# Performance work log

Measured on AMD Instinct MI355X. Metric: run time of the kernel, lower is better.

Reference implementation:

```python
import jax, jax.numpy as jnp
import numpy as np

BN_EPS = 1e-5
NUM_HEADS = 16


def setup_inputs() -> dict:
    key = jax.random.key(0)
    k1, k2 = jax.random.split(key)
    B, F, E = 8, 1024, 1024
    x = jax.random.normal(k1, (B, F, E), dtype=jnp.float32)
    # xavier_uniform for Linear(E, 3E): bound = sqrt(6/(E + 3E))
    bound = float(np.sqrt(6.0 / (E + 3 * E)))
    W_qkv = jax.random.uniform(k2, (3 * E, E), minval=-bound, maxval=bound, dtype=jnp.float32)
    b_qkv = jnp.zeros((3 * E,), dtype=jnp.float32)
    gamma = jnp.ones((F,), dtype=jnp.float32)
    beta = jnp.zeros((F,), dtype=jnp.float32)
    return {"x": x, "gamma": gamma, "beta": beta, "W_qkv": W_qkv, "b_qkv": b_qkv}


def reference(x, gamma, beta, W_qkv, b_qkv):
    B, F, E = x.shape
    H = NUM_HEADS
    hd = E // H
    # BatchNorm1d(features_dim) in training mode: channels = F axis,
    # stats over (batch, embed) dims, biased variance.
    mean = jnp.mean(x, axis=(0, 2), keepdims=True)          # [1,F,1]
    var = jnp.mean((x - mean) ** 2, axis=(0, 2), keepdims=True)
    xn = (x - mean) * jax.lax.rsqrt(var + BN_EPS)
    xn = xn * gamma[None, :, None] + beta[None, :, None]
    # QKV projection: torch Linear -> xn @ W^T + b
    qkv = jnp.einsum('bfe,oe->bfo', xn, W_qkv) + b_qkv       # [B,F,3E]
    qkv = qkv.reshape(B, F, H, 3 * hd).transpose(0, 2, 1, 3) # [B,H,F,3hd]
    q, k, v = jnp.split(qkv, 3, axis=-1)                     # each [B,H,F,hd]
    scale = 1.0 / jnp.sqrt(jnp.float32(hd))
    logits = jnp.einsum('bhqd,bhkd->bhqk', q, k) * scale     # [B,H,F,F]
    attn = jax.nn.softmax(logits, axis=-1)
    values = jnp.einsum('bhqk,bhkd->bhqd', attn, v)          # [B,H,F,hd]
    values = values.transpose(0, 2, 1, 3).reshape(B, F, E)
    return values
```

## Files before the change

kernel.cpp:

```cpp
#include <hip/hip_runtime.h>

typedef unsigned short u16;
typedef unsigned int   u32;

typedef __bf16 bf16x8 __attribute__((ext_vector_type(8)));
typedef float  f32x4  __attribute__((ext_vector_type(4)));

typedef const __attribute__((address_space(1))) void* gas_ptr;
typedef __attribute__((address_space(3))) void* las_ptr;

__device__ __forceinline__ u16 f2bf(float f) {
  u32 u = __builtin_bit_cast(u32, f);
  u += 0x7fffu + ((u >> 16) & 1u);
  return (u16)(u >> 16);
}
__device__ __forceinline__ float bf2f(u16 u) {
  return __builtin_bit_cast(float, ((u32)u) << 16);
}
__device__ __forceinline__ u32 pk2(float a, float b) {
  return (u32)f2bf(a) | ((u32)f2bf(b) << 16);
}

__global__ __launch_bounds__(256) void bn_norm_kernel(
    const float* __restrict__ x, const float* __restrict__ gamma,
    const float* __restrict__ beta, u16* __restrict__ xn) {
  const int F = 1024, E = 1024;
  int f = blockIdx.x;
  __shared__ float sh[8192];
  __shared__ float ps[4], pq[4], sc[2];

  const float* xf = x + (size_t)f * E;
  float ls = 0.f, lq = 0.f;
  for (int i = threadIdx.x; i < 8192; i += 256) {
    int b = i >> 10, e = i & 1023;
    float v = xf[(size_t)b * F * E + e];
    sh[i] = v;
    ls += v;
    lq += v * v;
  }
  #pragma unroll
  for (int o = 32; o > 0; o >>= 1) {
    ls += __shfl_down(ls, o, 64);
    lq += __shfl_down(lq, o, 64);
  }
  int w = threadIdx.x >> 6;
  if ((threadIdx.x & 63) == 0) { ps[w] = ls; pq[w] = lq; }
  __syncthreads();
  if (threadIdx.x == 0) {
    float s = ps[0] + ps[1] + ps[2] + ps[3];
    float q = pq[0] + pq[1] + pq[2] + pq[3];
    float mean = s * (1.f / 8192.f);
    float var = q * (1.f / 8192.f) - mean * mean;
    float scale = gamma[f] * rsqrtf(var + 1e-5f);
    sc[0] = scale;
    sc[1] = beta[f] - mean * scale;
  }
  __syncthreads();
  float scale = sc[0], shift = sc[1];
  for (int i = threadIdx.x; i < 8192; i += 256) {
    int b = i >> 10, e = i & 1023;
    xn[((size_t)(b * F + f)) * E + e] = f2bf(sh[i] * scale + shift);
  }
}

__global__ __launch_bounds__(256) void wconv_kernel(
    const float* __restrict__ W, u16* __restrict__ Wb) {
  const int total = 3072 * 1024 / 4;
  for (int i = blockIdx.x * 256 + threadIdx.x; i < total; i += gridDim.x * 256) {
    float4 v = ((const float4*)W)[i];
    ushort4 o;
    o.x = f2bf(v.x); o.y = f2bf(v.y); o.z = f2bf(v.z); o.w = f2bf(v.w);
    ((ushort4*)Wb)[i] = o;
  }
}

__global__ __launch_bounds__(256) void gemm_qkv_kernel(
    const u16* __restrict__ A, const u16* __restrict__ Bw,
    const float* __restrict__ bias, u16* __restrict__ C) {
  const int K = 1024, N = 3072;
  __shared__ u16 As[128 * 32];
  __shared__ u16 Bs[128 * 32];

  int m0 = blockIdx.x * 128, n0 = blockIdx.y * 128;
  int t = threadIdx.x, lane = t & 63, w = t >> 6;
  int wr = w >> 1, wc = w & 1;
  int r = lane & 15, g = lane >> 4;

  int srow = t >> 2, scol = (t & 3) * 8;
  const u16* gA  = A  + (size_t)(m0 + srow) * K + scol;
  const u16* gA2 = gA + (size_t)64 * K;
  const u16* gB  = Bw + (size_t)(n0 + srow) * K + scol;
  const u16* gB2 = gB + (size_t)64 * K;
  u16* lA  = As + t * 8;
  u16* lA2 = As + 2048 + t * 8;
  u16* lB  = Bs + t * 8;
  u16* lB2 = Bs + 2048 + t * 8;

  f32x4 acc[4][4] = {};

  const u16* pA = As + (size_t)(wr * 64 + r) * 32 + g * 8;
  const u16* pB = Bs + (size_t)(wc * 64 + r) * 32 + g * 8;

  for (int k0 = 0; k0 < K; k0 += 32) {
    __builtin_amdgcn_global_load_lds((gas_ptr)gA,  (las_ptr)lA,  16, 0, 0);
    __builtin_amdgcn_global_load_lds((gas_ptr)gA2, (las_ptr)lA2, 16, 0, 0);
    __builtin_amdgcn_global_load_lds((gas_ptr)gB,  (las_ptr)lB,  16, 0, 0);
    __builtin_amdgcn_global_load_lds((gas_ptr)gB2, (las_ptr)lB2, 16, 0, 0);
    gA += 32; gA2 += 32; gB += 32; gB2 += 32;
    __syncthreads();

    bf16x8 af[4], bfr[4];
    #pragma unroll
    for (int mi = 0; mi < 4; ++mi)
      af[mi] = __builtin_bit_cast(bf16x8, *(const int4*)(pA + mi * 512));
    #pragma unroll
    for (int ni = 0; ni < 4; ++ni)
      bfr[ni] = __builtin_bit_cast(bf16x8, *(const int4*)(pB + ni * 512));
    #pragma unroll
    for (int mi = 0; mi < 4; ++mi)
      #pragma unroll
      for (int ni = 0; ni < 4; ++ni)
        acc[mi][ni] = __builtin_amdgcn_mfma_f32_16x16x32_bf16(af[mi], bfr[ni], acc[mi][ni], 0, 0, 0);
    __syncthreads();
  }

  #pragma unroll
  for (int ni = 0; ni < 4; ++ni) {
    int col = n0 + wc * 64 + ni * 16 + r;
    float bv = bias[col];
    #pragma unroll
    for (int mi = 0; mi < 4; ++mi) {
      int row = m0 + wr * 64 + mi * 16 + g * 4;
      #pragma unroll
      for (int j = 0; j < 4; ++j)
        C[(size_t)(row + j) * N + col] = f2bf(acc[mi][ni][j] + bv);
    }
  }
}

__global__ __launch_bounds__(256) void vt_kernel(
    const u16* __restrict__ qkv, u16* __restrict__ Vt) {
  __shared__ u16 T[64][72];
  int bh = blockIdx.y, b = bh >> 4, h = bh & 15;
  int f0 = blockIdx.x * 64;
  int t = threadIdx.x;
  int fl = t >> 2, c16 = (t & 3) * 16;
  const u16* src = qkv + (size_t)(b * 1024 + f0 + fl) * 3072 + h * 192 + 128 + c16;
  *(int4*)&T[fl][c16]     = *(const int4*)src;
  *(int4*)&T[fl][c16 + 8] = *(const int4*)(src + 8);
  __syncthreads();
  int dl = t >> 2, fc = (t & 3) * 16;
  u16 buf[16];
  #pragma unroll
  for (int j = 0; j < 16; ++j) {
    int c = fc + j;
    int m = c & 31;
    int a = ((m & 4) << 2) | ((m & 16) >> 1) | ((m & 8) >> 1) | (m & 3);
    buf[j] = T[(c & 32) | a][dl];
  }
  u16* dst = Vt + (size_t)bh * 65536 + (size_t)dl * 1024 + f0 + fc;
  *(int4*)dst       = *(int4*)&buf[0];
  *(int4*)(dst + 8) = *(int4*)&buf[8];
}

__global__ __launch_bounds__(256) void attn_kernel(
    const u16* __restrict__ qkv, const u16* __restrict__ Vt,
    float* __restrict__ out) {
  const int F = 1024, NQ = 3072;
  int bid = blockIdx.x;
  int xcd = bid & 7;
  int li  = bid >> 3;
  int bh  = ((li >> 4) << 3) | xcd;
  int ql  = li & 15;
  int w   = threadIdx.x >> 6;
  int lane = threadIdx.x & 63;
  int q = lane & 15, g = lane >> 4;
  int qs = q & 7;
  int q0 = ql * 64 + w * 16;
  int b = bh >> 4, h = bh & 15;

  const u16* base = qkv + (size_t)b * F * NQ + h * 192;
  const u16* VtBH = Vt + (size_t)bh * 65536;

  __shared__ u16 S[16384];

  int i8 = lane >> 3;
  int ic = lane & 7;

  const float qscale = 0.125f * 1.4426950408889634f;
  bf16x8 Qf0, Qf1;
  {
    const u16* qp = base + (size_t)(q0 + q) * NQ + g * 8;
    union { int4 v; u16 u[8]; } uu0, uu1;
    uu0.v = *(const int4*)(qp);
    uu1.v = *(const int4*)(qp + 32);
    union { u16 u[8]; bf16x8 v; } p0, p1;
    #pragma unroll
    for (int j = 0; j < 8; ++j) {
      p0.u[j] = f2bf(bf2f(uu0.u[j]) * qscale);
      p1.u[j] = f2bf(bf2f(uu1.u[j]) * qscale);
    }
    Qf0 = p0.v; Qf1 = p1.v;
  }

  f32x4 acc[4] = {};
  float m = -INFINITY, lsum = 0.f;

  #define STAGE(buf, kt)                                                       \
    do {                                                                       \
      int kb_ = (kt) * 64;                                                     \
      _Pragma("unroll")                                                        \
      for (int rr = 0; rr < 2; ++rr) {                                         \
        int r_ = rr * 32 + w * 8 + i8;                                         \
        int sc_ = (ic ^ (r_ & 7)) * 8;                                         \
        const u16* ks_ = base + (size_t)(kb_ + r_) * NQ + 64 + sc_;            \
        const u16* vs_ = VtBH + (size_t)r_ * 1024 + kb_ + sc_;                 \
        __builtin_amdgcn_global_load_lds((gas_ptr)ks_,                         \
            (las_ptr)&S[(buf) * 4096 + (rr * 32 + w * 8) * 64], 16, 0, 0);     \
        __builtin_amdgcn_global_load_lds((gas_ptr)vs_,                         \
            (las_ptr)&S[8192 + (buf) * 4096 + (rr * 32 + w * 8) * 64], 16, 0, 0);\
      }                                                                        \
    } while (0)

  STAGE(0, 0);
  __syncthreads();

  int cur = 0;
  for (int kt = 0; kt < 16; ++kt) {
    if (kt < 15) STAGE(cur ^ 1, kt + 1);

    const u16* Kb = &S[cur * 4096];
    const u16* Vb = &S[8192 + cur * 4096];

    f32x4 s[4];
    #pragma unroll
    for (int ks = 0; ks < 4; ++ks) {
      int row = ks * 16 + q;
      int4 k0 = *(const int4*)&Kb[row * 64 + ((g ^ qs) * 8)];
      int4 k1 = *(const int4*)&Kb[row * 64 + (((4 + g) ^ qs) * 8)];
      f32x4 sv = {0.f, 0.f, 0.f, 0.f};
      sv = __builtin_amdgcn_mfma_f32_16x16x32_bf16(__builtin_bit_cast(bf16x8, k0), Qf0, sv, 0, 0, 0);
      sv = __builtin_amdgcn_mfma_f32_16x16x32_bf16(__builtin_bit_cast(bf16x8, k1), Qf1, sv, 0, 0, 0);
      s[ks] = sv;
    }

    float tmx = s[0][0];
    #pragma unroll
    for (int ks = 0; ks < 4; ++ks) {
      tmx = fmaxf(tmx, fmaxf(fmaxf(s[ks][0], s[ks][1]), fmaxf(s[ks][2], s[ks][3])));
    }
    if (__any(tmx > m + 8.0f)) {
      float tr = fmaxf(tmx, __shfl_xor(tmx, 16, 64));
      tr = fmaxf(tr, __shfl_xor(tr, 32, 64));
      float mnew = fmaxf(m, tr);
      float alpha = exp2f(m - mnew);
      lsum *= alpha;
      acc[0] *= alpha; acc[1] *= alpha; acc[2] *= alpha; acc[3] *= alpha;
      m = mnew;
    }
    float p[16];
    #pragma unroll
    for (int ks = 0; ks < 4; ++ks) {
      p[ks * 4 + 0] = exp2f(s[ks][0] - m);
      p[ks * 4 + 1] = exp2f(s[ks][1] - m);
      p[ks * 4 + 2] = exp2f(s[ks][2] - m);
      p[ks * 4 + 3] = exp2f(s[ks][3] - m);
    }
    float psum = 0.f;
    #pragma unroll
    for (int j = 0; j < 16; ++j) psum += p[j];
    lsum += psum;

    union { u32 w4[4]; bf16x8 v; } pb0, pb1;
    pb0.w4[0] = pk2(p[0], p[1]);   pb0.w4[1] = pk2(p[2], p[3]);
    pb0.w4[2] = pk2(p[4], p[5]);   pb0.w4[3] = pk2(p[6], p[7]);
    pb1.w4[0] = pk2(p[8], p[9]);   pb1.w4[1] = pk2(p[10], p[11]);
    pb1.w4[2] = pk2(p[12], p[13]); pb1.w4[3] = pk2(p[14], p[15]);

    #pragma unroll
    for (int dt = 0; dt < 4; ++dt) {
      int row = dt * 16 + q;
      int4 v0 = *(const int4*)&Vb[row * 64 + ((g ^ qs) * 8)];
      int4 v1 = *(const int4*)&Vb[row * 64 + (((4 + g) ^ qs) * 8)];
      acc[dt] = __builtin_amdgcn_mfma_f32_16x16x32_bf16(__builtin_bit_cast(bf16x8, v0), pb0.v, acc[dt], 0, 0, 0);
      acc[dt] = __builtin_amdgcn_mfma_f32_16x16x32_bf16(__builtin_bit_cast(bf16x8, v1), pb1.v, acc[dt], 0, 0, 0);
    }

    __syncthreads();
    cur ^= 1;
  }
  #undef STAGE

  lsum += __shfl_xor(lsum, 16, 64);
  lsum += __shfl_xor(lsum, 32, 64);
  float inv = 1.0f / lsum;

  float* oT = (float*)S + (size_t)w * 1088;
  #pragma unroll
  for (int dt = 0; dt < 4; ++dt) {
    oT[(dt * 16 + g * 4 + 0) * 17 + q] = acc[dt][0] * inv;
    oT[(dt * 16 + g * 4 + 1) * 17 + q] = acc[dt][1] * inv;
    oT[(dt * 16 + g * 4 + 2) * 17 + q] = acc[dt][2] * inv;
    oT[(dt * 16 + g * 4 + 3) * 17 + q] = acc[dt][3] * inv;
  }
  asm volatile("s_waitcnt lgkmcnt(0)" ::: "memory");
  int oq = lane >> 2, dc = (lane & 3) * 16;
  float* orow = out + (size_t)(b * F + q0 + oq) * 1024 + h * 64 + dc;
  #pragma unroll
  for (int c4 = 0; c4 < 4; ++c4) {
    float4 v;
    v.x = oT[(dc + c4 * 4 + 0) * 17 + oq];
    v.y = oT[(dc + c4 * 4 + 1) * 17 + oq];
    v.z = oT[(dc + c4 * 4 + 2) * 17 + oq];
    v.w = oT[(dc + c4 * 4 + 3) * 17 + oq];
    *(float4*)(orow + c4 * 4) = v;
  }
}

extern "C" void kernel_launch(void* const* d_in, const int* in_sizes, int n_in,
                              void* d_out, int out_size, void* d_ws, size_t ws_size,
                              hipStream_t stream) {
  const float* x     = (const float*)d_in[0];
  const float* gamma = (const float*)d_in[1];
  const float* beta  = (const float*)d_in[2];
  const float* W     = (const float*)d_in[3];
  const float* bias  = (const float*)d_in[4];
  float* out = (float*)d_out;

  char* ws = (char*)d_ws;
  u16* xn  = (u16*)ws;
  u16* Wb  = (u16*)(ws + (size_t)16 * 1024 * 1024);
  u16* qkv = (u16*)(ws + (size_t)22 * 1024 * 1024);
  u16* Vt  = (u16*)(ws + (size_t)70 * 1024 * 1024);

  bn_norm_kernel<<<1024, 256, 0, stream>>>(x, gamma, beta, xn);
  wconv_kernel<<<768, 256, 0, stream>>>(W, Wb);
  gemm_qkv_kernel<<<dim3(64, 24), 256, 0, stream>>>(xn, Wb, bias, qkv);
  vt_kernel<<<dim3(16, 128), 256, 0, stream>>>(qkv, Vt);
  attn_kernel<<<2048, 256, 0, stream>>>(qkv, Vt, out);
}
```

Baseline: 171.5 us.

## Fold running max into MFMA accumulator seed and use hardware bf16 pack

The attention inner loop now seeds the QK MFMA accumulator with -m, so scores arrive already shifted and the per-element subtraction before exp2 disappears in the common case. The rescale branch works on the offset relative to the current max and is marked unlikely. Software bf16 rounding is replaced by the v_cvt_pk_bf16_f32 instruction, the max and sum reductions become trees, and s_setprio is raised around the MFMA blocks. Together these aim to cut VALU work in the softmax, in exchange for inline asm and a max that now starts at 0 instead of -inf.

```diff
diff --git a/kernel.cpp b/kernel.cpp
--- a/kernel.cpp
+++ b/kernel.cpp
@@ -17,8 +17,10 @@
 __device__ __forceinline__ float bf2f(u16 u) {
   return __builtin_bit_cast(float, ((u32)u) << 16);
 }
-__device__ __forceinline__ u32 pk2(float a, float b) {
-  return (u32)f2bf(a) | ((u32)f2bf(b) << 16);
+__device__ __forceinline__ u32 cvtpk(float a, float b) {
+  u32 r;
+  asm("v_cvt_pk_bf16_f32 %0, %1, %2" : "=v"(r) : "v"(a), "v"(b));
+  return r;
 }
 
 __global__ __launch_bounds__(256) void bn_norm_kernel(
@@ -194,17 +196,17 @@
     union { int4 v; u16 u[8]; } uu0, uu1;
     uu0.v = *(const int4*)(qp);
     uu1.v = *(const int4*)(qp + 32);
-    union { u16 u[8]; bf16x8 v; } p0, p1;
-    #pragma unroll
-    for (int j = 0; j < 8; ++j) {
-      p0.u[j] = f2bf(bf2f(uu0.u[j]) * qscale);
-      p1.u[j] = f2bf(bf2f(uu1.u[j]) * qscale);
+    union { u32 w4[4]; bf16x8 v; } p0, p1;
+    #pragma unroll
+    for (int j = 0; j < 4; ++j) {
+      p0.w4[j] = cvtpk(bf2f(uu0.u[2 * j]) * qscale, bf2f(uu0.u[2 * j + 1]) * qscale);
+      p1.w4[j] = cvtpk(bf2f(uu1.u[2 * j]) * qscale, bf2f(uu1.u[2 * j + 1]) * qscale);
     }
     Qf0 = p0.v; Qf1 = p1.v;
   }
 
   f32x4 acc[4] = {};
-  float m = -INFINITY, lsum = 0.f;
+  float m = 0.0f, lsum = 0.f;
 
   #define STAGE(buf, kt)                                                       \
     do {                                                                       \
@@ -233,50 +235,65 @@
     const u16* Vb = &S[8192 + cur * 4096];
 
     f32x4 s[4];
+    f32x4 seed = {-m, -m, -m, -m};
+    __builtin_amdgcn_s_setprio(1);
     #pragma unroll
     for (int ks = 0; ks < 4; ++ks) {
       int row = ks * 16 + q;
       int4 k0 = *(const int4*)&Kb[row * 64 + ((g ^ qs) * 8)];
       int4 k1 = *(const int4*)&Kb[row * 64 + (((4 + g) ^ qs) * 8)];
-      f32x4 sv = {0.f, 0.f, 0.f, 0.f};
+      f32x4 sv = seed;
       sv = __builtin_amdgcn_mfma_f32_16x16x32_bf16(__builtin_bit_cast(bf16x8, k0), Qf0, sv, 0, 0, 0);
       sv = __builtin_amdgcn_mfma_f32_16x16x32_bf16(__builtin_bit_cast(bf16x8, k1), Qf1, sv, 0, 0, 0);
       s[ks] = sv;
     }
-
-    float tmx = s[0][0];
-    #pragma unroll
-    for (int ks = 0; ks < 4; ++ks) {
-      tmx = fmaxf(tmx, fmaxf(fmaxf(s[ks][0], s[ks][1]), fmaxf(s[ks][2], s[ks][3])));
-    }
-    if (__any(tmx > m + 8.0f)) {
+    __builtin_amdgcn_s_setprio(0);
+
+    float a0 = fmaxf(fmaxf(s[0][0], s[0][1]), s[0][2]);
+    float a1 = fmaxf(fmaxf(s[0][3], s[1][0]), s[1][1]);
+    float a2 = fmaxf(fmaxf(s[1][2], s[1][3]), s[2][0]);
+    float a3 = fmaxf(fmaxf(s[2][1], s[2][2]), s[2][3]);
+    float a4 = fmaxf(fmaxf(s[3][0], s[3][1]), s[3][2]);
+    float tmx = fmaxf(fmaxf(fmaxf(a0, a1), a2), fmaxf(fmaxf(a3, a4), s[3][3]));
+
+    float p[16];
+    if (__builtin_expect(__any(tmx > 8.0f), 0)) {
       float tr = fmaxf(tmx, __shfl_xor(tmx, 16, 64));
       tr = fmaxf(tr, __shfl_xor(tr, 32, 64));
-      float mnew = fmaxf(m, tr);
-      float alpha = exp2f(m - mnew);
+      float dm = fmaxf(tr, 0.f);
+      float alpha = exp2f(-dm);
       lsum *= alpha;
       acc[0] *= alpha; acc[1] *= alpha; acc[2] *= alpha; acc[3] *= alpha;
-      m = mnew;
-    }
-    float p[16];
-    #pragma unroll
-    for (int ks = 0; ks < 4; ++ks) {
-      p[ks * 4 + 0] = exp2f(s[ks][0] - m);
-      p[ks * 4 + 1] = exp2f(s[ks][1] - m);
-      p[ks * 4 + 2] = exp2f(s[ks][2] - m);
-      p[ks * 4 + 3] = exp2f(s[ks][3] - m);
-    }
-    float psum = 0.f;
-    #pragma unroll
-    for (int j = 0; j < 16; ++j) psum += p[j];
-    lsum += psum;
+      m += dm;
+      #pragma unroll
+      for (int ks = 0; ks < 4; ++ks) {
+        p[ks * 4 + 0] = exp2f(s[ks][0] - dm);
+        p[ks * 4 + 1] = exp2f(s[ks][1] - dm);
+        p[ks * 4 + 2] = exp2f(s[ks][2] - dm);
+        p[ks * 4 + 3] = exp2f(s[ks][3] - dm);
+      }
+    } else {
+      #pragma unroll
+      for (int ks = 0; ks < 4; ++ks) {
+        p[ks * 4 + 0] = exp2f(s[ks][0]);
+        p[ks * 4 + 1] = exp2f(s[ks][1]);
+        p[ks * 4 + 2] = exp2f(s[ks][2]);
+        p[ks * 4 + 3] = exp2f(s[ks][3]);
+      }
+    }
+    float q01 = p[0] + p[1],   q23 = p[2] + p[3];
+    float q45 = p[4] + p[5],   q67 = p[6] + p[7];
+    float q89 = p[8] + p[9],   qab = p[10] + p[11];
+    float qcd = p[12] + p[13], qef = p[14] + p[15];
+    lsum += ((q01 + q23) + (q45 + q67)) + ((q89 + qab) + (qcd + qef));
 
     union { u32 w4[4]; bf16x8 v; } pb0, pb1;
-    pb0.w4[0] = pk2(p[0], p[1]);   pb0.w4[1] = pk2(p[2], p[3]);
-    pb0.w4[2] = pk2(p[4], p[5]);   pb0.w4[3] = pk2(p[6], p[7]);
-    pb1.w4[0] = pk2(p[8], p[9]);   pb1.w4[1] = pk2(p[10], p[11]);
-    pb1.w4[2] = pk2(p[12], p[13]); pb1.w4[3] = pk2(p[14], p[15]);
-
+    pb0.w4[0] = cvtpk(p[0], p[1]);   pb0.w4[1] = cvtpk(p[2], p[3]);
+    pb0.w4[2] = cvtpk(p[4], p[5]);   pb0.w4[3] = cvtpk(p[6], p[7]);
+    pb1.w4[0] = cvtpk(p[8], p[9]);   pb1.w4[1] = cvtpk(p[10], p[11]);
+    pb1.w4[2] = cvtpk(p[12], p[13]); pb1.w4[3] = cvtpk(p[14], p[15]);
+
+    __builtin_amdgcn_s_setprio(1);
     #pragma unroll
     for (int dt = 0; dt < 4; ++dt) {
       int row = dt * 16 + q;
@@ -285,6 +302,7 @@
       acc[dt] = __builtin_amdgcn_mfma_f32_16x16x32_bf16(__builtin_bit_cast(bf16x8, v0), pb0.v, acc[dt], 0, 0, 0);
       acc[dt] = __builtin_amdgcn_mfma_f32_16x16x32_bf16(__builtin_bit_cast(bf16x8, v1), pb1.v, acc[dt], 0, 0, 0);
     }
+    __builtin_amdgcn_s_setprio(0);
 
     __syncthreads();
     cur ^= 1;
```

After: 167.7 us. 2.2% less time.
